# Kernel optimization log

Measured on AMD Instinct MI355X. Metric: run time of the kernel, lower is better.

The kernel has to match this reference:

```python
import jax, jax.numpy as jnp
import numpy as np

B, L, E, DA, R = 256, 2048, 64, 64, 32

def setup_inputs() -> dict:
    key = jax.random.key(0)
    k1, k2, k3, k4 = jax.random.split(key, 4)
    x = jax.random.normal(k1, (B, L, E), dtype=jnp.float32)
    mask = (jax.random.uniform(k2, (B, L)) > 0.2).astype(jnp.float32)
    # glorot-uniform-like init for the small attention weights
    lim1 = np.sqrt(6.0 / (DA + E)).astype(np.float32)
    lim2 = np.sqrt(6.0 / (R + DA)).astype(np.float32)
    W1 = jax.random.uniform(k3, (DA, E), minval=-lim1, maxval=lim1, dtype=jnp.float32)
    W2 = jax.random.uniform(k4, (R, DA), minval=-lim2, maxval=lim2, dtype=jnp.float32)
    return {"x": x, "mask": mask, "W1": W1, "W2": W2}

def reference(x, mask, W1, W2):
    # x: (B,L,E), mask: (B,L), W1: (DA,E), W2: (R,DA)
    xm = x * mask[:, :, None]                       # masked inputs (B,L,E)
    H = jnp.tanh(jnp.einsum('de,ble->bdl', W1, xm))  # (B,DA,L)
    Q = jnp.einsum('rd,bdl->brl', W2, H)             # (B,R,L)
    A = jnp.exp(Q) * mask[:, None, :]                # masked exp scores (B,R,L)
    A = A / jnp.sum(A, axis=2, keepdims=True)        # normalize over L
    # dropout is identity at inference
    return jnp.einsum('brl,ble->bre', A, xm)         # (B,R,E)
```

## Files before the change

kernel.cpp:

```cpp
#include <hip/hip_runtime.h>
#include <hip/hip_bf16.h>


#define B_  256
#define L_  2048
#define E_  64
#define DA_ 64
#define R_  32
#define CH_ 8
#define NS_ 4
#define TL_ 64

typedef __attribute__((ext_vector_type(8))) short bf16x8;
typedef __attribute__((ext_vector_type(4))) float f32x4;

#define HS_P 36
#define XT_P 36
#define AS_P 36
#define HS_W (64 * HS_P)
#define XT_W (64 * XT_P)
#define AS_W (32 * AS_P)

__device__ __forceinline__ unsigned pk(float a, float b) {
    __hip_bfloat162 h = __float22bfloat162_rn(float2{a, b});
    union { __hip_bfloat162 h2; unsigned u; } cv; cv.h2 = h;
    return cv.u;
}
__device__ __forceinline__ float bflo(unsigned u) { return __uint_as_float(u << 16); }
__device__ __forceinline__ float bfhi(unsigned u) { return __uint_as_float(u & 0xFFFF0000u); }
__device__ __forceinline__ float fast_tanh(float v) {
    float e = __builtin_amdgcn_exp2f(v * 2.885390082f);
    float r = __builtin_amdgcn_rcpf(e + 1.0f);
    return fmaf(-2.0f, r, 1.0f);
}
__device__ __forceinline__ float fast_exp(float v) {
    return __builtin_amdgcn_exp2f(v * 1.442695041f);
}

__launch_bounds__(256, 4)
__global__ void selfbi_main(const float* __restrict__ x,
                            const float* __restrict__ mask,
                            const float* __restrict__ W1,
                            const float* __restrict__ W2,
                            float* __restrict__ accp,
                            float* __restrict__ ssump) {
    __shared__ __align__(16) unsigned smem[HS_W + 2 * XT_W + 2 * AS_W + 128];
    unsigned* hsw  = smem;
    unsigned* xtw0 = smem + HS_W;
    unsigned* asw0 = xtw0 + 2 * XT_W;
    float*    ssl  = (float*)(asw0 + 2 * AS_W);

    const int b    = blockIdx.x;
    const int c    = blockIdx.y;
    const int tid  = threadIdx.x;
    const int w    = tid >> 6;
    const int lane = tid & 63;
    const int g    = lane >> 4;
    const int ml   = lane & 15;

    bf16x8 w1f[4][2], w2f[2][2];
    #pragma unroll
    for (int mt = 0; mt < 4; ++mt)
        #pragma unroll
        for (int kb = 0; kb < 2; ++kb) {
            const float* p = W1 + (16 * mt + ml) * E_ + 32 * kb + 8 * g;
            float4 a = *(const float4*)p, bb = *(const float4*)(p + 4);
            union { bf16x8 s; unsigned u[4]; } cv;
            cv.u[0] = pk(a.x, a.y); cv.u[1] = pk(a.z, a.w);
            cv.u[2] = pk(bb.x, bb.y); cv.u[3] = pk(bb.z, bb.w);
            w1f[mt][kb] = cv.s;
        }
    #pragma unroll
    for (int nt = 0; nt < 2; ++nt)
        #pragma unroll
        for (int kb = 0; kb < 2; ++kb) {
            const float* p = W2 + (16 * nt + ml) * DA_ + 32 * kb + 8 * g;
            float4 a = *(const float4*)p, bb = *(const float4*)(p + 4);
            union { bf16x8 s; unsigned u[4]; } cv;
            cv.u[0] = pk(a.x, a.y); cv.u[1] = pk(a.z, a.w);
            cv.u[2] = pk(bb.x, bb.y); cv.u[3] = pk(bb.z, bb.w);
            w2f[nt][kb] = cv.s;
        }

    f32x4 c3[2] = {f32x4{0,0,0,0}, f32x4{0,0,0,0}};
    float sswav0 = 0.0f, sswav1 = 0.0f;

    const int trow  = 16 * w + ml;
    const int thalf = trow >> 1, tbyte = trow & 1;
    const size_t cbase = ((size_t)b * L_ + c * (NS_ * TL_)) * E_;
    const int    mbase = b * L_ + c * (NS_ * TL_);

    float4 gx[2][2], mk;
    {
        const float* xr = x + cbase + (size_t)trow * E_ + 8 * g;
        gx[0][0] = *(const float4*)xr;
        gx[0][1] = *(const float4*)(xr + 4);
        gx[1][0] = *(const float4*)(xr + 32);
        gx[1][1] = *(const float4*)(xr + 36);
        mk = *(const float4*)(mask + mbase + 16 * w + 4 * g);
    }

    for (int s = 0; s < NS_; ++s) {
        unsigned* xtw = xtw0 + (s & 1) * XT_W;
        unsigned* asw = asw0 + (s & 1) * AS_W;

        bf16x8 xf[2];
        union { bf16x8 s; unsigned u[4]; } xc[2];
        #pragma unroll
        for (int kb = 0; kb < 2; ++kb) {
            xc[kb].u[0] = pk(gx[kb][0].x, gx[kb][0].y);
            xc[kb].u[1] = pk(gx[kb][0].z, gx[kb][0].w);
            xc[kb].u[2] = pk(gx[kb][1].x, gx[kb][1].y);
            xc[kb].u[3] = pk(gx[kb][1].z, gx[kb][1].w);
            xf[kb] = xc[kb].s;
        }

        float4 gxn[2][2], mkn;
        if (s + 1 < NS_) {
            const float* xr = x + cbase + (size_t)((s + 1) * TL_ + trow) * E_ + 8 * g;
            gxn[0][0] = *(const float4*)xr;
            gxn[0][1] = *(const float4*)(xr + 4);
            gxn[1][0] = *(const float4*)(xr + 32);
            gxn[1][1] = *(const float4*)(xr + 36);
            mkn = *(const float4*)(mask + mbase + (s + 1) * TL_ + 16 * w + 4 * g);
        }

        #pragma unroll
        for (int kb = 0; kb < 2; ++kb)
            #pragma unroll
            for (int i = 0; i < 4; ++i) {
                const int e0 = 32 * kb + 8 * g + 2 * i;
                const int wd = thalf ^ (8 * g);
                ((unsigned short*)&xtw[e0 * XT_P + wd])[tbyte] =
                    (unsigned short)(xc[kb].u[i] & 0xFFFF);
                ((unsigned short*)&xtw[(e0 + 1) * XT_P + wd])[tbyte] =
                    (unsigned short)(xc[kb].u[i] >> 16);
            }

        f32x4 c1[4] = {f32x4{0,0,0,0}, f32x4{0,0,0,0}, f32x4{0,0,0,0}, f32x4{0,0,0,0}};
        #pragma unroll
        for (int kb = 0; kb < 2; ++kb)
            #pragma unroll
            for (int mt = 0; mt < 4; ++mt)
                c1[mt] = __builtin_amdgcn_mfma_f32_16x16x32_bf16(
                    w1f[mt][kb], xf[kb], c1[mt], 0, 0, 0);

        #pragma unroll
        for (int mt = 0; mt < 4; ++mt) {
            float h0 = fast_tanh(c1[mt][0]);
            float h1 = fast_tanh(c1[mt][1]);
            float h2 = fast_tanh(c1[mt][2]);
            float h3 = fast_tanh(c1[mt][3]);
            uint2 u; u.x = pk(h0, h1); u.y = pk(h2, h3);
            *(uint2*)&hsw[trow * HS_P + 8 * mt + 2 * g] = u;
        }

        f32x4 c2[2] = {f32x4{0,0,0,0}, f32x4{0,0,0,0}};
        #pragma unroll
        for (int kb = 0; kb < 2; ++kb) {
            bf16x8 af = *(bf16x8*)&hsw[trow * HS_P + 16 * kb + 4 * g];
            #pragma unroll
            for (int nt = 0; nt < 2; ++nt)
                c2[nt] = __builtin_amdgcn_mfma_f32_16x16x32_bf16(
                    af, w2f[nt][kb], c2[nt], 0, 0, 0);
        }

        float part0, part1;
        {
            const int tw = 8 * w + 2 * g;
            float a0 = fast_exp(c2[0][0]) * mk.x;
            float a1 = fast_exp(c2[0][1]) * mk.y;
            float a2 = fast_exp(c2[0][2]) * mk.z;
            float a3 = fast_exp(c2[0][3]) * mk.w;
            uint2 u; u.x = pk(a0, a1); u.y = pk(a2, a3);
            *(uint2*)&asw[ml * AS_P + tw] = u;
            part0 = bflo(u.x) + bfhi(u.x) + bflo(u.y) + bfhi(u.y);
            a0 = fast_exp(c2[1][0]) * mk.x;
            a1 = fast_exp(c2[1][1]) * mk.y;
            a2 = fast_exp(c2[1][2]) * mk.z;
            a3 = fast_exp(c2[1][3]) * mk.w;
            u.x = pk(a0, a1); u.y = pk(a2, a3);
            *(uint2*)&asw[(16 + ml) * AS_P + tw] = u;
            part1 = bflo(u.x) + bfhi(u.x) + bflo(u.y) + bfhi(u.y);
        }
        part0 += __shfl_xor(part0, 16); part0 += __shfl_xor(part0, 32);
        part1 += __shfl_xor(part1, 16); part1 += __shfl_xor(part1, 32);
        sswav0 += part0; sswav1 += part1;

        __syncthreads();

        {
            const int erow = 16 * w + ml;
            const int esw  = 8 * ((erow >> 3) & 3);
            #pragma unroll
            for (int kb = 0; kb < 2; ++kb) {
                bf16x8 bf = *(bf16x8*)&xtw[erow * XT_P + ((16 * kb + 4 * g) ^ esw)];
                #pragma unroll
                for (int mt = 0; mt < 2; ++mt) {
                    bf16x8 af = *(bf16x8*)&asw[(16 * mt + ml) * AS_P + 16 * kb + 4 * g];
                    c3[mt] = __builtin_amdgcn_mfma_f32_16x16x32_bf16(af, bf, c3[mt], 0, 0, 0);
                }
            }
        }

        gx[0][0] = gxn[0][0]; gx[0][1] = gxn[0][1];
        gx[1][0] = gxn[1][0]; gx[1][1] = gxn[1][1];
        mk = mkn;
    }

    const size_t obase = (size_t)(b * CH_ + c) * (R_ * E_);
    const int e = 16 * w + ml;
    #pragma unroll
    for (int mt = 0; mt < 2; ++mt)
        #pragma unroll
        for (int reg = 0; reg < 4; ++reg) {
            const int r = 16 * mt + 4 * g + reg;
            accp[obase + r * E_ + e] = c3[mt][reg];
        }
    if (g == 0) {
        ssl[w * 32 + ml]      = sswav0;
        ssl[w * 32 + 16 + ml] = sswav1;
    }
    __syncthreads();
    if (tid < 32)
        ssump[(b * CH_ + c) * R_ + tid] =
            ssl[tid] + ssl[32 + tid] + ssl[64 + tid] + ssl[96 + tid];
}

__launch_bounds__(256, 4)
__global__ void selfbi_reduce(const float* __restrict__ accp,
                              const float* __restrict__ ssump,
                              float* __restrict__ out) {
    const int of = blockIdx.x * 256 + threadIdx.x;
    const int b  = of >> 11;
    const int o  = of & 2047;
    const int r  = o >> 6;
    float num = 0.f, den = 0.f;
    #pragma unroll
    for (int cc = 0; cc < CH_; ++cc) {
        num += accp[((size_t)(b * CH_ + cc)) * (R_ * E_) + o];
        den += ssump[(b * CH_ + cc) * R_ + r];
    }
    out[of] = num / den;
}

extern "C" void kernel_launch(void* const* d_in, const int* in_sizes, int n_in,
                              void* d_out, int out_size, void* d_ws, size_t ws_size,
                              hipStream_t stream) {
    const float* x    = (const float*)d_in[0];
    const float* mask = (const float*)d_in[1];
    const float* W1   = (const float*)d_in[2];
    const float* W2   = (const float*)d_in[3];
    float* out        = (float*)d_out;

    float* accp  = (float*)d_ws;
    float* ssump = accp + (size_t)B_ * CH_ * R_ * E_;

    selfbi_main<<<dim3(B_, CH_), dim3(256), 0, stream>>>(x, mask, W1, W2, accp, ssump);
    selfbi_reduce<<<dim3((B_ * R_ * E_) / 256), dim3(256), 0, stream>>>(accp, ssump, out);
}
```

Baseline: 207.7 us.

## Permute H layout for vector stores, hoist sum shuffles, use fewer larger chunks

Halves the number of L-chunks per batch while doubling the sub-tiles each block processes. This gives fewer blocks, each amortizing weight setup over more work, and shrinks the partial-result reduction. The tanh outputs are now written to shared memory as two 128-bit stores instead of four 64-bit ones. The W2 fragment loading is permuted over the DA dimension to match the new H layout, which is valid because the contraction is order-independent. The cross-lane shuffle reduction of the softmax denominators moves out of the loop to run once per block, at the cost of less parallelism from the reduced grid size.

New measurement: 207.3 us. Within noise of the previous version (-0.2%).

```diff
diff --git a/kernel.cpp b/kernel.cpp
--- a/kernel.cpp
+++ b/kernel.cpp
@@ -7,8 +7,8 @@
 #define E_  64
 #define DA_ 64
 #define R_  32
-#define CH_ 8
-#define NS_ 4
+#define CH_ 4
+#define NS_ 8
 #define TL_ 64
 
 typedef __attribute__((ext_vector_type(8))) short bf16x8;
@@ -58,7 +58,7 @@
     const int g    = lane >> 4;
     const int ml   = lane & 15;
 
-    bf16x8 w1f[4][2], w2f[2][2];
+    bf16x8 w1f[4][2];
     #pragma unroll
     for (int mt = 0; mt < 4; ++mt)
         #pragma unroll
@@ -70,12 +70,15 @@
             cv.u[2] = pk(bb.x, bb.y); cv.u[3] = pk(bb.z, bb.w);
             w1f[mt][kb] = cv.s;
         }
+    bf16x8 w2f[2][2];
     #pragma unroll
     for (int nt = 0; nt < 2; ++nt)
         #pragma unroll
         for (int kb = 0; kb < 2; ++kb) {
-            const float* p = W2 + (16 * nt + ml) * DA_ + 32 * kb + 8 * g;
-            float4 a = *(const float4*)p, bb = *(const float4*)(p + 4);
+            const int dbase = 32 * (g & 1) + 4 * (2 * kb + (g >> 1));
+            const float* p = W2 + (16 * nt + ml) * DA_ + dbase;
+            float4 a  = *(const float4*)p;
+            float4 bb = *(const float4*)(p + 16);
             union { bf16x8 s; unsigned u[4]; } cv;
             cv.u[0] = pk(a.x, a.y); cv.u[1] = pk(a.z, a.w);
             cv.u[2] = pk(bb.x, bb.y); cv.u[3] = pk(bb.z, bb.w);
@@ -145,14 +148,20 @@
                 c1[mt] = __builtin_amdgcn_mfma_f32_16x16x32_bf16(
                     w1f[mt][kb], xf[kb], c1[mt], 0, 0, 0);
 
-        #pragma unroll
-        for (int mt = 0; mt < 4; ++mt) {
-            float h0 = fast_tanh(c1[mt][0]);
-            float h1 = fast_tanh(c1[mt][1]);
-            float h2 = fast_tanh(c1[mt][2]);
-            float h3 = fast_tanh(c1[mt][3]);
-            uint2 u; u.x = pk(h0, h1); u.y = pk(h2, h3);
-            *(uint2*)&hsw[trow * HS_P + 8 * mt + 2 * g] = u;
+        {
+            float th[4][4];
+            #pragma unroll
+            for (int mt = 0; mt < 4; ++mt)
+                #pragma unroll
+                for (int reg = 0; reg < 4; ++reg)
+                    th[mt][reg] = fast_tanh(c1[mt][reg]);
+            uint4 ua, ub;
+            ua.x = pk(th[0][0], th[0][1]); ua.y = pk(th[0][2], th[0][3]);
+            ua.z = pk(th[1][0], th[1][1]); ua.w = pk(th[1][2], th[1][3]);
+            ub.x = pk(th[2][0], th[2][1]); ub.y = pk(th[2][2], th[2][3]);
+            ub.z = pk(th[3][0], th[3][1]); ub.w = pk(th[3][2], th[3][3]);
+            *(uint4*)&hsw[trow * HS_P + 8 * g]     = ua;
+            *(uint4*)&hsw[trow * HS_P + 8 * g + 4] = ub;
         }
 
         f32x4 c2[2] = {f32x4{0,0,0,0}, f32x4{0,0,0,0}};
@@ -165,7 +174,6 @@
                     af, w2f[nt][kb], c2[nt], 0, 0, 0);
         }
 
-        float part0, part1;
         {
             const int tw = 8 * w + 2 * g;
             float a0 = fast_exp(c2[0][0]) * mk.x;
@@ -174,18 +182,15 @@
             float a3 = fast_exp(c2[0][3]) * mk.w;
             uint2 u; u.x = pk(a0, a1); u.y = pk(a2, a3);
             *(uint2*)&asw[ml * AS_P + tw] = u;
-            part0 = bflo(u.x) + bfhi(u.x) + bflo(u.y) + bfhi(u.y);
+            sswav0 += bflo(u.x) + bfhi(u.x) + bflo(u.y) + bfhi(u.y);
             a0 = fast_exp(c2[1][0]) * mk.x;
             a1 = fast_exp(c2[1][1]) * mk.y;
             a2 = fast_exp(c2[1][2]) * mk.z;
             a3 = fast_exp(c2[1][3]) * mk.w;
             u.x = pk(a0, a1); u.y = pk(a2, a3);
             *(uint2*)&asw[(16 + ml) * AS_P + tw] = u;
-            part1 = bflo(u.x) + bfhi(u.x) + bflo(u.y) + bfhi(u.y);
-        }
-        part0 += __shfl_xor(part0, 16); part0 += __shfl_xor(part0, 32);
-        part1 += __shfl_xor(part1, 16); part1 += __shfl_xor(part1, 32);
-        sswav0 += part0; sswav1 += part1;
+            sswav1 += bflo(u.x) + bfhi(u.x) + bflo(u.y) + bfhi(u.y);
+        }
 
         __syncthreads();
 
@@ -207,6 +212,9 @@
         gx[1][0] = gxn[1][0]; gx[1][1] = gxn[1][1];
         mk = mkn;
     }
+
+    sswav0 += __shfl_xor(sswav0, 16); sswav0 += __shfl_xor(sswav0, 32);
+    sswav1 += __shfl_xor(sswav1, 16); sswav1 += __shfl_xor(sswav1, 32);
 
     const size_t obase = (size_t)(b * CH_ + c) * (R_ * E_);
     const int e = 16 * w + ml;
```
